# Optimization experiments

Hardware: AMD Instinct MI355X
Metric: run time of the kernel (lower is better)

## Reference

```python
import jax, jax.numpy as jnp
import numpy as np

B, N, D, F, L, R = 16, 1024, 256, 128, 2, 2


def setup_inputs() -> dict:
    key = jax.random.key(0)
    ks = jax.random.split(key, 12)
    s = 0.05
    return {
        "node_embed": jax.random.normal(ks[0], (B, N, D), jnp.float32),
        "input_x": jax.random.normal(ks[1], (B, F), jnp.float32),
        "adj": jax.random.randint(ks[2], (R, B, N, N), 0, 2, jnp.int32),
        "WQi_w": jax.random.normal(ks[3], (L, F, F), jnp.float32) * s,
        "WQi_b": jnp.zeros((L, F), jnp.float32),
        "WQ_w": jax.random.normal(ks[4], (L, D + F, D), jnp.float32) * s,
        "WQ_b": jnp.zeros((L, D), jnp.float32),
        "WK_w": jax.random.normal(ks[5], (L, R, D + F, D), jnp.float32) * s,
        "WK_b": jnp.zeros((L, R, D), jnp.float32),
        "WV_w": jax.random.normal(ks[6], (L, R, D + F, D), jnp.float32) * s,
        "WV_b": jnp.zeros((L, R, D), jnp.float32),
        "WF_w": jax.random.normal(ks[7], (L, R * D, D), jnp.float32) * s,
        "WF_b": jnp.zeros((L, D), jnp.float32),
        "ln_g": jnp.ones((L, D), jnp.float32),
        "ln_b": jnp.zeros((L, D), jnp.float32),
    }


def _layer_norm(x, g, b, eps=1e-5):
    mu = jnp.mean(x, axis=-1, keepdims=True)
    var = jnp.var(x, axis=-1, keepdims=True)
    return (x - mu) * jax.lax.rsqrt(var + eps) * g + b


def reference(node_embed, input_x, adj, WQi_w, WQi_b, WQ_w, WQ_b,
              WK_w, WK_b, WV_w, WV_b, WF_w, WF_b, ln_g, ln_b):
    scale = 1.0 / (D ** 0.5)
    h = node_embed
    for l in range(L):
        # input feature projection, broadcast over nodes
        x1 = input_x @ WQi_w[l] + WQi_b[l]              # (B, F)
        x1 = jnp.broadcast_to(x1[:, None, :], (h.shape[0], h.shape[1], F))
        qc = jnp.concatenate([h, x1], axis=-1)          # (B, N, D+F)
        q = qc @ WQ_w[l] + WQ_b[l]                      # (B, N, D)
        outs = []
        for r in range(R):
            k = qc @ WK_w[l, r] + WK_b[l, r]            # (B, N, D)
            v = qc @ WV_w[l, r] + WV_b[l, r]            # (B, N, D)
            scores = jnp.einsum('bnd,bmd->bnm', q, k) * scale
            scores = jnp.where(adj[r] == 0, -1e9, scores)
            alpha = jax.nn.softmax(scores, axis=-1)
            outs.append(jnp.einsum('bnm,bmd->bnd', alpha, v))
        h_concat = jnp.concatenate(outs, axis=-1)       # (B, N, R*D)
        h_fused = jax.nn.relu(h_concat @ WF_w[l] + WF_b[l])
        h = _layer_norm(h + h_fused, ln_g[l], ln_b[l])
    return h
```

## Files before the change

kernel.cpp:

```cpp
#include <hip/hip_runtime.h>
#include <hip/hip_bf16.h>

#define BB 16
#define NN 1024
#define DD 256
#define FF_ 128
#define LL 2
#define RR 2
#define DF 384
#define MM (BB*NN)
#define NPROJ 1280

typedef __attribute__((ext_vector_type(8))) short s16x8;
typedef __attribute__((ext_vector_type(4))) float f32x4;

__device__ __forceinline__ unsigned short f2bf(float f){
  unsigned u = __builtin_bit_cast(unsigned, f);
  u += 0x7fff + ((u >> 16) & 1);
  return (unsigned short)(u >> 16);
}

__device__ __forceinline__ void gload16(const void* g, void* l){
  __builtin_amdgcn_global_load_lds(
      (const __attribute__((address_space(1))) unsigned int*)g,
      (__attribute__((address_space(3))) unsigned int*)l, 16, 0, 0);
}

#define MFMA16(a,b,c) __builtin_amdgcn_mfma_f32_16x16x32_bf16((a),(b),(c),0,0,0)

__global__ __launch_bounds__(256) void pack_adj(const int* __restrict__ adj,
                                                unsigned long long* __restrict__ bits){
  int w = threadIdx.x >> 6, lane = threadIdx.x & 63;
  size_t row = (size_t)blockIdx.x * 4 + w;
  const int* a = adj + row * NN;
  unsigned long long* brow = bits + row * 16;
  #pragma unroll
  for (int j = 0; j < 16; ++j){
    unsigned long long m = __ballot(a[j*64 + lane] != 0);
    if (lane == 0) brow[j] = m;
  }
}

__global__ void x1_proj(const float* __restrict__ x, const float* __restrict__ wq,
                        const float* __restrict__ bq, float* __restrict__ x1){
  int b = blockIdx.x, j = threadIdx.x;
  float s = bq[j];
  for (int i = 0; i < FF_; ++i) s += x[b*FF_ + i] * wq[i*FF_ + j];
  x1[b*FF_ + j] = s;
}

__global__ void w_to_bf16T(const float* __restrict__ in, unsigned short* __restrict__ out, int K){
  int o = blockIdx.x * 256 + threadIdx.x;
  int n = o / K, k = o - n*K;
  out[o] = f2bf(in[(size_t)k * 256 + n]);
}

__global__ void wcat(const float* __restrict__ WQ, const float* __restrict__ WK,
                     const float* __restrict__ WV, unsigned short* __restrict__ wt){
  int o = blockIdx.x * 256 + threadIdx.x;
  int n = o / DF, k = o - n*DF;
  float v;
  if (n < 256)      v = WQ[(size_t)k*256 + n];
  else if (n < 768) v = WK[(size_t)((n-256)>>8)*(DF*256) + (size_t)k*256 + ((n-256)&255)];
  else              v = WV[(size_t)((n-768)>>8)*(DF*256) + (size_t)k*256 + ((n-768)&255)];
  wt[o] = f2bf(v);
}

__global__ void bcat(const float* __restrict__ bq, const float* __restrict__ bk,
                     const float* __restrict__ bv, float* __restrict__ ball){
  int n = blockIdx.x * 256 + threadIdx.x;
  if (n >= NPROJ) return;
  ball[n] = (n < 256) ? bq[n] : (n < 768) ? bk[n-256] : bv[n-768];
}

__global__ __launch_bounds__(256) void qc_h(const float* __restrict__ h, unsigned short* __restrict__ qc){
  int o = blockIdx.x * 256 + threadIdx.x;
  int m = o >> 8, c = o & 255;
  qc[(size_t)m * DF + c] = f2bf(h[o]);
}

__global__ __launch_bounds__(256) void qc_x1(const float* __restrict__ x1, unsigned short* __restrict__ qc){
  int m = blockIdx.x * 2 + (threadIdx.x >> 7);
  int c = threadIdx.x & 127;
  qc[(size_t)m * DF + 256 + c] = f2bf(x1[(m >> 10) * FF_ + c]);
}

template<int OUTF32>
__global__ __launch_bounds__(256) void gemm2(const unsigned short* __restrict__ A, int lda,
    const unsigned short* __restrict__ Wt, const float* __restrict__ bias,
    void* __restrict__ out, int ldo, int nk){
  __shared__ unsigned short As[2][128*32];
  __shared__ unsigned short Bs[2][128*32];
  int t = threadIdx.x, lane = t & 63, w = t >> 6;
  int wr = w >> 1, wc = w & 1, l15 = lane & 15, lhi = lane >> 4;
  int bm = blockIdx.x, bn = blockIdx.y;
  f32x4 acc[4][4];
  #pragma unroll
  for (int m = 0; m < 4; ++m)
    #pragma unroll
    for (int n = 0; n < 4; ++n) acc[m][n] = (f32x4){0.f,0.f,0.f,0.f};

  auto STAGE = [&](int bufi, int kk){
    #pragma unroll
    for (int i = 0; i < 2; ++i){
      int base = w*2048 + i*1024;
      int off = base + lane*16;
      int row = off >> 6, cb = off & 63;
      gload16((const char*)A  + ((size_t)(bm*128 + row)*lda + kk*32)*2 + cb,
              (char*)As[bufi] + base);
      gload16((const char*)Wt + ((size_t)(bn*128 + row)*DF  + 0)*0 + ((size_t)(bn*128 + row)*lda + kk*32)*2 + cb,
              (char*)Bs[bufi] + base);
    }
  };

  STAGE(0, 0);
  __syncthreads();
  for (int kk = 0; kk < nk; ++kk){
    int cur = kk & 1;
    if (kk + 1 < nk) STAGE(cur ^ 1, kk + 1);
    s16x8 af[4], bfr[4];
    #pragma unroll
    for (int m = 0; m < 4; ++m) af[m]  = *(const s16x8*)&As[cur][(wr*64 + m*16 + l15)*32 + lhi*8];
    #pragma unroll
    for (int n = 0; n < 4; ++n) bfr[n] = *(const s16x8*)&Bs[cur][(wc*64 + n*16 + l15)*32 + lhi*8];
    #pragma unroll
    for (int m = 0; m < 4; ++m)
      #pragma unroll
      for (int n = 0; n < 4; ++n)
        acc[m][n] = MFMA16(af[m], bfr[n], acc[m][n]);
    __syncthreads();
  }

  #pragma unroll
  for (int n = 0; n < 4; ++n){
    int gn = bn*128 + wc*64 + n*16 + l15;
    float bv = bias[gn];
    #pragma unroll
    for (int m = 0; m < 4; ++m){
      int gm = bm*128 + wr*64 + m*16 + lhi*4;
      #pragma unroll
      for (int i = 0; i < 4; ++i){
        float v = acc[m][n][i] + bv;
        size_t o = (size_t)(gm + i) * ldo + gn;
        if (OUTF32) ((float*)out)[o] = v;
        else        ((unsigned short*)out)[o] = f2bf(v);
      }
    }
  }
}

__global__ __launch_bounds__(256) void transpose2(const unsigned short* __restrict__ P,
                                                  unsigned short* __restrict__ vt){
  __shared__ unsigned short tl[64][66];
  int z = blockIdx.z;
  int b = z & 15, r = z >> 4;
  int n0 = blockIdx.x*64, d0 = blockIdx.y*64;
  int t = threadIdx.x;
  #pragma unroll
  for (int it = 0; it < 16; ++it){
    int idx = t + it*256;
    int rr = idx >> 6, cc = idx & 63;
    tl[rr][cc] = P[(size_t)(b*NN + n0 + rr)*NPROJ + 768 + r*256 + d0 + cc];
  }
  __syncthreads();
  #pragma unroll
  for (int it = 0; it < 16; ++it){
    int idx = t + it*256;
    int rr = idx >> 6, cc = idx & 63;
    vt[((size_t)z*256 + d0 + rr)*NN + n0 + cc] = tl[cc][rr];
  }
}

__global__ __launch_bounds__(512, 2) void attn2(const unsigned short* __restrict__ P,
    const unsigned short* __restrict__ VT, const unsigned long long* __restrict__ bits,
    unsigned short* __restrict__ hc){
  __shared__ unsigned short Kt[64*256];
  __shared__ unsigned short Vt[256*64];
  __shared__ unsigned short Pl[8][16*72];
  int t = threadIdx.x, lane = t & 63, w = t >> 6, l15 = lane & 15, lhi = lane >> 4;
  int F = blockIdx.x;
  int xcd = F & 7, j = F >> 3;
  int qt = j & 7;
  int gidx = xcd*4 + (j >> 3);
  int b = gidx & 15, r = gidx >> 4;
  const float scale = 0.0625f;

  const unsigned short* Qb = P;
  size_t kcol = 256 + (size_t)r*256;
  const unsigned short* Vb = VT + ((size_t)(r*16 + b))*256*NN;

  s16x8 qf[8];
  {
    int qrow = qt*128 + w*16 + l15;
    const unsigned short* qp = Qb + ((size_t)(b*NN + qrow))*NPROJ + lhi*8;
    #pragma unroll
    for (int dc = 0; dc < 8; ++dc) qf[dc] = *(const s16x8*)(qp + dc*32);
  }

  f32x4 acc[16];
  #pragma unroll
  for (int i = 0; i < 16; ++i) acc[i] = (f32x4){0.f,0.f,0.f,0.f};
  float mrow[4] = {-1e30f,-1e30f,-1e30f,-1e30f};
  float lrow[4] = {0.f,0.f,0.f,0.f};
  size_t bitrow = ((size_t)(r*BB + b))*NN + qt*128 + w*16 + lhi*4;

  for (int kt = 0; kt < 16; ++kt){
    __syncthreads();
    #pragma unroll
    for (int i = 0; i < 4; ++i){
      int base = w*4096 + i*512;
      int off = base + lane*16;
      (void)off;
    }
    #pragma unroll
    for (int i = 0; i < 4; ++i){
      int base = w*4096 + i*1024;
      int off = base + lane*16;
      int row = off >> 9, cb = off & 511;
      int scb = cb ^ ((row & 7) << 4);
      gload16((const char*)P + ((size_t)(b*NN + kt*64 + row)*NPROJ + kcol)*2 + scb,
              (char*)Kt + base);
    }
    #pragma unroll
    for (int i = 0; i < 4; ++i){
      int base = w*4096 + i*1024;
      int off = base + lane*16;
      int row = off >> 7, cb = off & 127;
      int scb = cb ^ ((row & 7) << 4);
      gload16((const char*)Vb + ((size_t)row*NN + kt*64)*2 + scb,
              (char*)Vt + base);
    }
    __syncthreads();

    f32x4 sf[4];
    #pragma unroll
    for (int ks = 0; ks < 4; ++ks){
      sf[ks] = (f32x4){0.f,0.f,0.f,0.f};
      int krow = ks*16 + l15;
      #pragma unroll
      for (int dc = 0; dc < 8; ++dc){
        int bo = krow*512 + (((dc*32 + lhi*8)*2) ^ ((krow & 7) << 4));
        s16x8 kf = *(const s16x8*)((const char*)Kt + bo);
        sf[ks] = MFMA16(qf[dc], kf, sf[ks]);
      }
    }

    unsigned short* pw = &Pl[w][0];
    #pragma unroll
    for (int i = 0; i < 4; ++i){
      unsigned long long mwv = bits[(bitrow + i)*16 + kt];
      float sv[4]; float tm = -1e30f;
      #pragma unroll
      for (int ks = 0; ks < 4; ++ks){
        float s = sf[ks][i] * scale;
        bool on = (mwv >> (ks*16 + l15)) & 1ULL;
        s = on ? s : -1e9f;
        sv[ks] = s;
        tm = fmaxf(tm, s);
      }
      #pragma unroll
      for (int xm = 1; xm < 16; xm <<= 1) tm = fmaxf(tm, __shfl_xor(tm, xm));
      float mn = fmaxf(mrow[i], tm);
      float f = __expf(mrow[i] - mn);
      mrow[i] = mn;
      float rs = 0.f;
      #pragma unroll
      for (int ks = 0; ks < 4; ++ks){
        float e = __expf(sv[ks] - mn);
        pw[(lhi*4 + i)*72 + ks*16 + l15] = f2bf(e);
        rs += e;
      }
      #pragma unroll
      for (int xm = 1; xm < 16; xm <<= 1) rs += __shfl_xor(rs, xm);
      lrow[i] = lrow[i]*f + rs;
      #pragma unroll
      for (int dt = 0; dt < 16; ++dt) acc[dt][i] *= f;
    }

    s16x8 pa[2];
    #pragma unroll
    for (int kc = 0; kc < 2; ++kc)
      pa[kc] = *(const s16x8*)&pw[l15*72 + kc*32 + lhi*8];

    #pragma unroll
    for (int dt = 0; dt < 16; ++dt){
      int vrow = dt*16 + l15;
      #pragma unroll
      for (int kc = 0; kc < 2; ++kc){
        int bo = vrow*128 + (((kc*32 + lhi*8)*2) ^ ((vrow & 7) << 4));
        s16x8 vf = *(const s16x8*)((const char*)Vt + bo);
        acc[dt] = MFMA16(pa[kc], vf, acc[dt]);
      }
    }
  }

  #pragma unroll
  for (int i = 0; i < 4; ++i){
    float inv = 1.f / lrow[i];
    int q = qt*128 + w*16 + lhi*4 + i;
    unsigned short* hrow = hc + ((size_t)(b*NN + q))*(RR*DD) + r*DD;
    #pragma unroll
    for (int dt = 0; dt < 16; ++dt)
      hrow[dt*16 + l15] = f2bf(acc[dt][i] * inv);
  }
}

template<int WRITEQC>
__global__ __launch_bounds__(256) void ln_res2(const float* __restrict__ ff,
    const float* __restrict__ hin, const float* __restrict__ g,
    const float* __restrict__ bv, float* __restrict__ hout,
    unsigned short* __restrict__ qc){
  int w = threadIdx.x >> 6, lane = threadIdx.x & 63;
  size_t row = (size_t)blockIdx.x * 4 + w;
  f32x4 fv = *(const f32x4*)(ff  + row*DD + lane*4);
  f32x4 hv = *(const f32x4*)(hin + row*DD + lane*4);
  float x[4], s = 0.f, ss = 0.f;
  #pragma unroll
  for (int j = 0; j < 4; ++j){ x[j] = fmaxf(fv[j], 0.f) + hv[j]; s += x[j]; ss += x[j]*x[j]; }
  #pragma unroll
  for (int xm = 1; xm < 64; xm <<= 1){ s += __shfl_xor(s, xm); ss += __shfl_xor(ss, xm); }
  float mu = s * (1.f/256.f);
  float var = ss * (1.f/256.f) - mu*mu;
  float rstd = rsqrtf(var + 1e-5f);
  f32x4 o;
  #pragma unroll
  for (int j = 0; j < 4; ++j){ int c = lane*4 + j; o[j] = (x[j]-mu)*rstd*g[c] + bv[c]; }
  *(f32x4*)(hout + row*DD + lane*4) = o;
  if (WRITEQC){
    unsigned v0 = (unsigned)f2bf(o[0]) | ((unsigned)f2bf(o[1]) << 16);
    unsigned v1 = (unsigned)f2bf(o[2]) | ((unsigned)f2bf(o[3]) << 16);
    uint2 pv; pv.x = v0; pv.y = v1;
    *(uint2*)(qc + row*DF + lane*4) = pv;
  }
}

extern "C" void kernel_launch(void* const* d_in, const int* in_sizes, int n_in,
                              void* d_out, int out_size, void* d_ws, size_t ws_size,
                              hipStream_t stream){
  (void)in_sizes; (void)n_in; (void)out_size; (void)ws_size;
  const float* node  = (const float*)d_in[0];
  const float* inx   = (const float*)d_in[1];
  const int*   adj   = (const int*)d_in[2];
  const float* WQi_w = (const float*)d_in[3];
  const float* WQi_b = (const float*)d_in[4];
  const float* WQ_w  = (const float*)d_in[5];
  const float* WQ_b  = (const float*)d_in[6];
  const float* WK_w  = (const float*)d_in[7];
  const float* WK_b  = (const float*)d_in[8];
  const float* WV_w  = (const float*)d_in[9];
  const float* WV_b  = (const float*)d_in[10];
  const float* WF_w  = (const float*)d_in[11];
  const float* WF_b  = (const float*)d_in[12];
  const float* ln_g  = (const float*)d_in[13];
  const float* ln_b  = (const float*)d_in[14];
  float* hout = (float*)d_out;

  char* wsp = (char*)d_ws;
  auto alloc = [&](size_t n){ char* p = wsp; wsp += (n + 255) & ~(size_t)255; return p; };
  unsigned long long* bits = (unsigned long long*)alloc((size_t)RR*BB*NN*16*8);
  unsigned short* qc    = (unsigned short*)alloc((size_t)MM*DF*2);
  float*          x1    = (float*)alloc((size_t)BB*FF_*4);
  unsigned short* wtall = (unsigned short*)alloc((size_t)NPROJ*DF*2);
  float*          ball  = (float*)alloc((size_t)NPROJ*4);
  unsigned short* wtf   = (unsigned short*)alloc((size_t)DD*512*2);
  unsigned short* POUT  = (unsigned short*)alloc((size_t)MM*NPROJ*2);
  unsigned short* vtall = (unsigned short*)alloc((size_t)RR*BB*DD*NN*2);
  unsigned short* hc    = (unsigned short*)alloc((size_t)MM*512*2);
  float*          ffo   = (float*)alloc((size_t)MM*DD*4);

  pack_adj<<<RR*BB*NN/4, 256, 0, stream>>>(adj, bits);

  for (int l = 0; l < LL; ++l){
    x1_proj<<<BB, FF_, 0, stream>>>(inx, WQi_w + (size_t)l*FF_*FF_, WQi_b + l*FF_, x1);
    qc_x1<<<MM/2, 256, 0, stream>>>(x1, qc);
    if (l == 0) qc_h<<<MM, 256, 0, stream>>>(node, qc);

    wcat<<<NPROJ*DF/256, 256, 0, stream>>>(WQ_w + (size_t)l*DF*DD,
                                           WK_w + (size_t)l*RR*DF*DD,
                                           WV_w + (size_t)l*RR*DF*DD, wtall);
    bcat<<<5, 256, 0, stream>>>(WQ_b + l*DD, WK_b + (size_t)l*RR*DD, WV_b + (size_t)l*RR*DD, ball);
    w_to_bf16T<<<512, 256, 0, stream>>>(WF_w + (size_t)l*512*DD, wtf, 512);

    gemm2<0><<<dim3(128,10), 256, 0, stream>>>(qc, DF, wtall, ball, POUT, NPROJ, DF/32);

    transpose2<<<dim3(16,4,RR*BB), 256, 0, stream>>>(POUT, vtall);

    attn2<<<256, 512, 0, stream>>>(POUT, vtall, bits, hc);

    gemm2<1><<<dim3(128,2), 256, 0, stream>>>(hc, 512, wtf, WF_b + l*DD, ffo, DD, 512/32);

    const float* hsrc = l ? (const float*)hout : node;
    if (l == 0) ln_res2<1><<<MM/4, 256, 0, stream>>>(ffo, hsrc, ln_g, ln_b, hout, qc);
    else        ln_res2<0><<<MM/4, 256, 0, stream>>>(ffo, hsrc, ln_g + DD, ln_b + DD, hout, qc);
  }
}
```

Before: 344.2 us.

## Fuse prep kernels, write V transposed from GEMM, double-buffer attention tiles

```diff
diff --git a/kernel.cpp b/kernel.cpp
--- a/kernel.cpp
+++ b/kernel.cpp
@@ -10,9 +10,11 @@
 #define DF 384
 #define MM (BB*NN)
 #define NPROJ 1280
+#define PK 768
 
 typedef __attribute__((ext_vector_type(8))) short s16x8;
 typedef __attribute__((ext_vector_type(4))) float f32x4;
+typedef __attribute__((ext_vector_type(4))) unsigned short us16x4;
 
 __device__ __forceinline__ unsigned short f2bf(float f){
   unsigned u = __builtin_bit_cast(unsigned, f);
@@ -41,54 +43,298 @@
   }
 }
 
-__global__ void x1_proj(const float* __restrict__ x, const float* __restrict__ wq,
-                        const float* __restrict__ bq, float* __restrict__ x1){
-  int b = blockIdx.x, j = threadIdx.x;
-  float s = bq[j];
-  for (int i = 0; i < FF_; ++i) s += x[b*FF_ + i] * wq[i*FF_ + j];
-  x1[b*FF_ + j] = s;
-}
-
-__global__ void w_to_bf16T(const float* __restrict__ in, unsigned short* __restrict__ out, int K){
-  int o = blockIdx.x * 256 + threadIdx.x;
-  int n = o / K, k = o - n*K;
-  out[o] = f2bf(in[(size_t)k * 256 + n]);
-}
-
-__global__ void wcat(const float* __restrict__ WQ, const float* __restrict__ WK,
-                     const float* __restrict__ WV, unsigned short* __restrict__ wt){
-  int o = blockIdx.x * 256 + threadIdx.x;
-  int n = o / DF, k = o - n*DF;
-  float v;
-  if (n < 256)      v = WQ[(size_t)k*256 + n];
-  else if (n < 768) v = WK[(size_t)((n-256)>>8)*(DF*256) + (size_t)k*256 + ((n-256)&255)];
-  else              v = WV[(size_t)((n-768)>>8)*(DF*256) + (size_t)k*256 + ((n-768)&255)];
-  wt[o] = f2bf(v);
-}
-
-__global__ void bcat(const float* __restrict__ bq, const float* __restrict__ bk,
-                     const float* __restrict__ bv, float* __restrict__ ball){
-  int n = blockIdx.x * 256 + threadIdx.x;
-  if (n >= NPROJ) return;
-  ball[n] = (n < 256) ? bq[n] : (n < 768) ? bk[n-256] : bv[n-768];
-}
-
-__global__ __launch_bounds__(256) void qc_h(const float* __restrict__ h, unsigned short* __restrict__ qc){
-  int o = blockIdx.x * 256 + threadIdx.x;
-  int m = o >> 8, c = o & 255;
-  qc[(size_t)m * DF + c] = f2bf(h[o]);
-}
-
-__global__ __launch_bounds__(256) void qc_x1(const float* __restrict__ x1, unsigned short* __restrict__ qc){
-  int m = blockIdx.x * 2 + (threadIdx.x >> 7);
-  int c = threadIdx.x & 127;
-  qc[(size_t)m * DF + 256 + c] = f2bf(x1[(m >> 10) * FF_ + c]);
-}
-
-template<int OUTF32>
-__global__ __launch_bounds__(256) void gemm2(const unsigned short* __restrict__ A, int lda,
+#define PREP_WT   3840
+#define PREP_WTF  1024
+#define PREP_BALL 10
+#define PREP_X1   16
+#define PREP_H    2048
+#define PREP_TOT  (PREP_WT+PREP_WTF+PREP_BALL+PREP_X1+PREP_H)
+
+__global__ __launch_bounds__(256) void prep(
+    const float* __restrict__ node, const float* __restrict__ inx,
+    const float* __restrict__ WQi_w, const float* __restrict__ WQi_b,
+    const float* __restrict__ WQ_w, const float* __restrict__ WK_w,
+    const float* __restrict__ WV_w, const float* __restrict__ WQ_b,
+    const float* __restrict__ WK_b, const float* __restrict__ WV_b,
+    const float* __restrict__ WF_w,
+    unsigned short* __restrict__ wtall, unsigned short* __restrict__ wtf,
+    float* __restrict__ ball, unsigned short* __restrict__ x1bf,
+    unsigned short* __restrict__ hbf){
+  int bid = blockIdx.x, t = threadIdx.x;
+  if (bid < PREP_WT){
+    int o = bid*256 + t;
+    int l = o / (NPROJ*DF); int oo = o - l*(NPROJ*DF);
+    int n = oo / DF, k = oo - n*DF;
+    const float* WQ = WQ_w + (size_t)l*DF*256;
+    const float* WK = WK_w + (size_t)l*RR*DF*256;
+    const float* WV = WV_w + (size_t)l*RR*DF*256;
+    float v;
+    if (n < 256)      v = WQ[(size_t)k*256 + n];
+    else if (n < 768) v = WK[(size_t)((n-256)>>8)*(DF*256) + (size_t)k*256 + ((n-256)&255)];
+    else              v = WV[(size_t)((n-768)>>8)*(DF*256) + (size_t)k*256 + ((n-768)&255)];
+    wtall[o] = f2bf(v);
+  } else if (bid < PREP_WT + PREP_WTF){
+    int o = (bid - PREP_WT)*256 + t;
+    int l = o >> 17; int oo = o & 131071;
+    int n = oo >> 9, k = oo & 511;
+    wtf[o] = f2bf(WF_w[(size_t)l*512*256 + (size_t)k*256 + n]);
+  } else if (bid < PREP_WT + PREP_WTF + PREP_BALL){
+    int o = (bid - PREP_WT - PREP_WTF)*256 + t;
+    if (o < 2*NPROJ){
+      int l = o / NPROJ, n = o - l*NPROJ;
+      float v = (n < 256) ? WQ_b[l*256 + n]
+              : (n < 768) ? WK_b[(size_t)l*512 + (n-256)]
+                          : WV_b[(size_t)l*512 + (n-768)];
+      ball[o] = v;
+    }
+  } else if (bid < PREP_WT + PREP_WTF + PREP_BALL + PREP_X1){
+    int o = (bid - PREP_WT - PREP_WTF - PREP_BALL)*256 + t;
+    int l = o >> 11, bj = o & 2047;
+    int b = bj >> 7, j = bj & 127;
+    const float* w = WQi_w + (size_t)l*FF_*FF_;
+    float s = WQi_b[l*FF_ + j];
+    for (int i = 0; i < FF_; ++i) s += inx[b*FF_ + i] * w[i*FF_ + j];
+    x1bf[o] = f2bf(s);
+  } else {
+    int o = (bid - (PREP_TOT - PREP_H))*256 + t;
+    const float4* src = (const float4*)node + (size_t)o*2;
+    float4 a = src[0], c = src[1];
+    uint4 pk;
+    pk.x = (unsigned)f2bf(a.x) | ((unsigned)f2bf(a.y) << 16);
+    pk.y = (unsigned)f2bf(a.z) | ((unsigned)f2bf(a.w) << 16);
+    pk.z = (unsigned)f2bf(c.x) | ((unsigned)f2bf(c.y) << 16);
+    pk.w = (unsigned)f2bf(c.z) | ((unsigned)f2bf(c.w) << 16);
+    *(uint4*)(hbf + (size_t)o*8) = pk;
+  }
+}
+
+__global__ __launch_bounds__(256) void gemm_big(const unsigned short* __restrict__ hbf,
+    const unsigned short* __restrict__ x1l, const unsigned short* __restrict__ Wt,
+    const float* __restrict__ bias, unsigned short* __restrict__ POUT,
+    unsigned short* __restrict__ vtall){
+  __shared__ unsigned short As[2][128*32];
+  __shared__ unsigned short Bs[2][128*32];
+  int t = threadIdx.x, lane = t & 63, w = t >> 6;
+  int wr = w >> 1, wc = w & 1, l15 = lane & 15, lhi = lane >> 4;
+  int bm = blockIdx.x, bn = blockIdx.y, bb = bm >> 3;
+  f32x4 acc[4][4];
+  #pragma unroll
+  for (int m = 0; m < 4; ++m)
+    #pragma unroll
+    for (int n = 0; n < 4; ++n) acc[m][n] = (f32x4){0.f,0.f,0.f,0.f};
+
+  auto STAGE = [&](int bi, int kk){
+    #pragma unroll
+    for (int i = 0; i < 2; ++i){
+      int base = w*2048 + i*1024;
+      int off = base + lane*16;
+      int row = off >> 6, cb = off & 63;
+      const char* asrc = (kk < 8)
+        ? (const char*)hbf + ((size_t)(bm*128 + row)*256 + kk*32)*2 + cb
+        : (const char*)x1l + ((size_t)bb*128 + (kk-8)*32)*2 + cb;
+      gload16(asrc, (char*)As[bi] + base);
+      gload16((const char*)Wt + ((size_t)(bn*128 + row)*DF + kk*32)*2 + cb,
+              (char*)Bs[bi] + base);
+    }
+  };
+
+  STAGE(0, 0);
+  __syncthreads();
+  for (int kk = 0; kk < 12; ++kk){
+    int cur = kk & 1;
+    if (kk + 1 < 12) STAGE(cur ^ 1, kk + 1);
+    s16x8 af[4], bfr[4];
+    #pragma unroll
+    for (int m = 0; m < 4; ++m) af[m]  = *(const s16x8*)&As[cur][(wr*64 + m*16 + l15)*32 + lhi*8];
+    #pragma unroll
+    for (int n = 0; n < 4; ++n) bfr[n] = *(const s16x8*)&Bs[cur][(wc*64 + n*16 + l15)*32 + lhi*8];
+    __builtin_amdgcn_s_setprio(1);
+    #pragma unroll
+    for (int m = 0; m < 4; ++m)
+      #pragma unroll
+      for (int n = 0; n < 4; ++n)
+        acc[m][n] = MFMA16(af[m], bfr[n], acc[m][n]);
+    __builtin_amdgcn_s_setprio(0);
+    __syncthreads();
+  }
+
+  if (bn < 6){
+    #pragma unroll
+    for (int n = 0; n < 4; ++n){
+      int gn = bn*128 + wc*64 + n*16 + l15;
+      float bv = bias[gn];
+      #pragma unroll
+      for (int m = 0; m < 4; ++m){
+        int gm = bm*128 + wr*64 + m*16 + lhi*4;
+        #pragma unroll
+        for (int i = 0; i < 4; ++i)
+          POUT[(size_t)(gm + i)*PK + gn] = f2bf(acc[m][n][i] + bv);
+      }
+    }
+  } else {
+    #pragma unroll
+    for (int n = 0; n < 4; ++n){
+      int gn = bn*128 + wc*64 + n*16 + l15;
+      float bv = bias[gn];
+      int rv = gn - 768;
+      int r = rv >> 8, d = rv & 255;
+      #pragma unroll
+      for (int m = 0; m < 4; ++m){
+        int mb = (bm & 7)*128 + wr*64 + m*16 + lhi*4;
+        us16x4 pk;
+        #pragma unroll
+        for (int i = 0; i < 4; ++i) pk[i] = f2bf(acc[m][n][i] + bv);
+        *(us16x4*)(vtall + ((size_t)((r*16 + bb)*256 + d))*NN + mb) = pk;
+      }
+    }
+  }
+}
+
+__global__ __launch_bounds__(512, 2) void attn2(const unsigned short* __restrict__ P,
+    const unsigned short* __restrict__ VT, const unsigned long long* __restrict__ bits,
+    unsigned short* __restrict__ hc){
+  __shared__ unsigned short Kt[2][64*256];
+  __shared__ unsigned short Vt[2][256*64];
+  __shared__ unsigned short Pl[8][16*68];
+  int t = threadIdx.x, lane = t & 63, w = t >> 6, l15 = lane & 15, lhi = lane >> 4;
+  int F = blockIdx.x;
+  int xcd = F & 7, j = F >> 3;
+  int qt = j & 7;
+  int gidx = xcd*4 + (j >> 3);
+  int b = gidx & 15, r = gidx >> 4;
+  const float C = 0.09016844f;
+
+  size_t kcol = 256 + (size_t)r*256;
+  const unsigned short* Vb = VT + ((size_t)(r*16 + b))*256*NN;
+
+  s16x8 qf[8];
+  {
+    int qrow = qt*128 + w*16 + l15;
+    const unsigned short* qp = P + ((size_t)(b*NN + qrow))*PK + lhi*8;
+    #pragma unroll
+    for (int dc = 0; dc < 8; ++dc) qf[dc] = *(const s16x8*)(qp + dc*32);
+  }
+
+  f32x4 acc[16];
+  #pragma unroll
+  for (int i = 0; i < 16; ++i) acc[i] = (f32x4){0.f,0.f,0.f,0.f};
+  float mrow[4] = {-3e38f,-3e38f,-3e38f,-3e38f};
+  float lrow[4] = {0.f,0.f,0.f,0.f};
+  size_t bitrow = ((size_t)(r*BB + b))*NN + qt*128 + w*16 + lhi*4;
+
+  auto STAGE = [&](int bi, int kt){
+    #pragma unroll
+    for (int i = 0; i < 4; ++i){
+      int base = w*4096 + i*1024;
+      int off = base + lane*16;
+      int row = off >> 9, cb = off & 511;
+      int scb = cb ^ ((row & 7) << 4);
+      gload16((const char*)P + ((size_t)(b*NN + kt*64 + row)*PK + kcol)*2 + scb,
+              (char*)Kt[bi] + base);
+    }
+    #pragma unroll
+    for (int i = 0; i < 4; ++i){
+      int base = w*4096 + i*1024;
+      int off = base + lane*16;
+      int row = off >> 7, cb = off & 127;
+      int scb = cb ^ ((row & 7) << 4);
+      gload16((const char*)Vb + ((size_t)row*NN + kt*64)*2 + scb,
+              (char*)Vt[bi] + base);
+    }
+  };
+
+  STAGE(0, 0);
+  __syncthreads();
+
+  for (int kt = 0; kt < 16; ++kt){
+    int cur = kt & 1;
+    if (kt + 1 < 16) STAGE(cur ^ 1, kt + 1);
+
+    f32x4 sf[4];
+    #pragma unroll
+    for (int ks = 0; ks < 4; ++ks){
+      sf[ks] = (f32x4){0.f,0.f,0.f,0.f};
+      int krow = ks*16 + l15;
+      __builtin_amdgcn_s_setprio(1);
+      #pragma unroll
+      for (int dc = 0; dc < 8; ++dc){
+        int bo = krow*512 + (((dc*32 + lhi*8)*2) ^ ((krow & 7) << 4));
+        s16x8 kf = *(const s16x8*)((const char*)Kt[cur] + bo);
+        sf[ks] = MFMA16(qf[dc], kf, sf[ks]);
+      }
+      __builtin_amdgcn_s_setprio(0);
+    }
+
+    unsigned short* pw = &Pl[w][0];
+    #pragma unroll
+    for (int i = 0; i < 4; ++i){
+      unsigned long long mwv = bits[(bitrow + i)*16 + kt];
+      float sv[4]; float tm = -3e38f;
+      #pragma unroll
+      for (int ks = 0; ks < 4; ++ks){
+        float s = sf[ks][i] * C;
+        bool on = (mwv >> (ks*16 + l15)) & 1ULL;
+        s = on ? s : -1.443e9f;
+        sv[ks] = s;
+        tm = fmaxf(tm, s);
+      }
+      #pragma unroll
+      for (int xm = 1; xm < 16; xm <<= 1) tm = fmaxf(tm, __shfl_xor(tm, xm));
+      float mn = mrow[i];
+      if (tm > mn + 11.6f){
+        float f = exp2f(mn - tm);
+        mrow[i] = tm; mn = tm;
+        lrow[i] *= f;
+        #pragma unroll
+        for (int dt = 0; dt < 16; ++dt) acc[dt][i] *= f;
+      }
+      float rs = 0.f;
+      #pragma unroll
+      for (int ks = 0; ks < 4; ++ks){
+        float e = exp2f(sv[ks] - mn);
+        pw[(lhi*4 + i)*68 + ks*16 + l15] = f2bf(e);
+        rs += e;
+      }
+      #pragma unroll
+      for (int xm = 1; xm < 16; xm <<= 1) rs += __shfl_xor(rs, xm);
+      lrow[i] += rs;
+    }
+
+    s16x8 pa[2];
+    #pragma unroll
+    for (int kc = 0; kc < 2; ++kc)
+      pa[kc] = *(const s16x8*)&pw[l15*68 + kc*32 + lhi*8];
+
+    __builtin_amdgcn_s_setprio(1);
+    #pragma unroll
+    for (int dt = 0; dt < 16; ++dt){
+      int vrow = dt*16 + l15;
+      #pragma unroll
+      for (int kc = 0; kc < 2; ++kc){
+        int bo = vrow*128 + (((kc*32 + lhi*8)*2) ^ ((vrow & 7) << 4));
+        s16x8 vf = *(const s16x8*)((const char*)Vt[cur] + bo);
+        acc[dt] = MFMA16(pa[kc], vf, acc[dt]);
+      }
+    }
+    __builtin_amdgcn_s_setprio(0);
+
+    __syncthreads();
+  }
+
+  #pragma unroll
+  for (int i = 0; i < 4; ++i){
+    float inv = 1.f / lrow[i];
+    int q = qt*128 + w*16 + lhi*4 + i;
+    unsigned short* hrow = hc + ((size_t)(b*NN + q))*(RR*DD) + r*DD;
+    #pragma unroll
+    for (int dt = 0; dt < 16; ++dt)
+      hrow[dt*16 + l15] = f2bf(acc[dt][i] * inv);
+  }
+}
+
+__global__ __launch_bounds__(256) void gemm_ff(const unsigned short* __restrict__ A,
     const unsigned short* __restrict__ Wt, const float* __restrict__ bias,
-    void* __restrict__ out, int ldo, int nk){
+    float* __restrict__ out){
   __shared__ unsigned short As[2][128*32];
   __shared__ unsigned short Bs[2][128*32];
   int t = threadIdx.x, lane = t & 63, w = t >> 6;
@@ -100,34 +346,36 @@
     #pragma unroll
     for (int n = 0; n < 4; ++n) acc[m][n] = (f32x4){0.f,0.f,0.f,0.f};
 
-  auto STAGE = [&](int bufi, int kk){
+  auto STAGE = [&](int bi, int kk){
     #pragma unroll
     for (int i = 0; i < 2; ++i){
       int base = w*2048 + i*1024;
       int off = base + lane*16;
       int row = off >> 6, cb = off & 63;
-      gload16((const char*)A  + ((size_t)(bm*128 + row)*lda + kk*32)*2 + cb,
-              (char*)As[bufi] + base);
-      gload16((const char*)Wt + ((size_t)(bn*128 + row)*DF  + 0)*0 + ((size_t)(bn*128 + row)*lda + kk*32)*2 + cb,
-              (char*)Bs[bufi] + base);
+      gload16((const char*)A  + ((size_t)(bm*128 + row)*512 + kk*32)*2 + cb,
+              (char*)As[bi] + base);
+      gload16((const char*)Wt + ((size_t)(bn*128 + row)*512 + kk*32)*2 + cb,
+              (char*)Bs[bi] + base);
     }
   };
 
   STAGE(0, 0);
   __syncthreads();
-  for (int kk = 0; kk < nk; ++kk){
+  for (int kk = 0; kk < 16; ++kk){
     int cur = kk & 1;
-    if (kk + 1 < nk) STAGE(cur ^ 1, kk + 1);
+    if (kk + 1 < 16) STAGE(cur ^ 1, kk + 1);
     s16x8 af[4], bfr[4];
     #pragma unroll
     for (int m = 0; m < 4; ++m) af[m]  = *(const s16x8*)&As[cur][(wr*64 + m*16 + l15)*32 + lhi*8];
     #pragma unroll
     for (int n = 0; n < 4; ++n) bfr[n] = *(const s16x8*)&Bs[cur][(wc*64 + n*16 + l15)*32 + lhi*8];
+    __builtin_amdgcn_s_setprio(1);
     #pragma unroll
     for (int m = 0; m < 4; ++m)
       #pragma unroll
       for (int n = 0; n < 4; ++n)
         acc[m][n] = MFMA16(af[m], bfr[n], acc[m][n]);
+    __builtin_amdgcn_s_setprio(0);
     __syncthreads();
   }
 
@@ -139,177 +387,17 @@
     for (int m = 0; m < 4; ++m){
       int gm = bm*128 + wr*64 + m*16 + lhi*4;
       #pragma unroll
-      for (int i = 0; i < 4; ++i){
-        float v = acc[m][n][i] + bv;
-        size_t o = (size_t)(gm + i) * ldo + gn;
-        if (OUTF32) ((float*)out)[o] = v;
-        else        ((unsigned short*)out)[o] = f2bf(v);
-      }
-    }
-  }
-}
-
-__global__ __launch_bounds__(256) void transpose2(const unsigned short* __restrict__ P,
-                                                  unsigned short* __restrict__ vt){
-  __shared__ unsigned short tl[64][66];
-  int z = blockIdx.z;
-  int b = z & 15, r = z >> 4;
-  int n0 = blockIdx.x*64, d0 = blockIdx.y*64;
-  int t = threadIdx.x;
-  #pragma unroll
-  for (int it = 0; it < 16; ++it){
-    int idx = t + it*256;
-    int rr = idx >> 6, cc = idx & 63;
-    tl[rr][cc] = P[(size_t)(b*NN + n0 + rr)*NPROJ + 768 + r*256 + d0 + cc];
-  }
-  __syncthreads();
-  #pragma unroll
-  for (int it = 0; it < 16; ++it){
-    int idx = t + it*256;
-    int rr = idx >> 6, cc = idx & 63;
-    vt[((size_t)z*256 + d0 + rr)*NN + n0 + cc] = tl[cc][rr];
-  }
-}
-
-__global__ __launch_bounds__(512, 2) void attn2(const unsigned short* __restrict__ P,
-    const unsigned short* __restrict__ VT, const unsigned long long* __restrict__ bits,
-    unsigned short* __restrict__ hc){
-  __shared__ unsigned short Kt[64*256];
-  __shared__ unsigned short Vt[256*64];
-  __shared__ unsigned short Pl[8][16*72];
-  int t = threadIdx.x, lane = t & 63, w = t >> 6, l15 = lane & 15, lhi = lane >> 4;
-  int F = blockIdx.x;
-  int xcd = F & 7, j = F >> 3;
-  int qt = j & 7;
-  int gidx = xcd*4 + (j >> 3);
-  int b = gidx & 15, r = gidx >> 4;
-  const float scale = 0.0625f;
-
-  const unsigned short* Qb = P;
-  size_t kcol = 256 + (size_t)r*256;
-  const unsigned short* Vb = VT + ((size_t)(r*16 + b))*256*NN;
-
-  s16x8 qf[8];
-  {
-    int qrow = qt*128 + w*16 + l15;
-    const unsigned short* qp = Qb + ((size_t)(b*NN + qrow))*NPROJ + lhi*8;
-    #pragma unroll
-    for (int dc = 0; dc < 8; ++dc) qf[dc] = *(const s16x8*)(qp + dc*32);
-  }
-
-  f32x4 acc[16];
-  #pragma unroll
-  for (int i = 0; i < 16; ++i) acc[i] = (f32x4){0.f,0.f,0.f,0.f};
-  float mrow[4] = {-1e30f,-1e30f,-1e30f,-1e30f};
-  float lrow[4] = {0.f,0.f,0.f,0.f};
-  size_t bitrow = ((size_t)(r*BB + b))*NN + qt*128 + w*16 + lhi*4;
-
-  for (int kt = 0; kt < 16; ++kt){
-    __syncthreads();
-    #pragma unroll
-    for (int i = 0; i < 4; ++i){
-      int base = w*4096 + i*512;
-      int off = base + lane*16;
-      (void)off;
-    }
-    #pragma unroll
-    for (int i = 0; i < 4; ++i){
-      int base = w*4096 + i*1024;
-      int off = base + lane*16;
-      int row = off >> 9, cb = off & 511;
-      int scb = cb ^ ((row & 7) << 4);
-      gload16((const char*)P + ((size_t)(b*NN + kt*64 + row)*NPROJ + kcol)*2 + scb,
-              (char*)Kt + base);
-    }
-    #pragma unroll
-    for (int i = 0; i < 4; ++i){
-      int base = w*4096 + i*1024;
-      int off = base + lane*16;
-      int row = off >> 7, cb = off & 127;
-      int scb = cb ^ ((row & 7) << 4);
-      gload16((const char*)Vb + ((size_t)row*NN + kt*64)*2 + scb,
-              (char*)Vt + base);
-    }
-    __syncthreads();
-
-    f32x4 sf[4];
-    #pragma unroll
-    for (int ks = 0; ks < 4; ++ks){
-      sf[ks] = (f32x4){0.f,0.f,0.f,0.f};
-      int krow = ks*16 + l15;
-      #pragma unroll
-      for (int dc = 0; dc < 8; ++dc){
-        int bo = krow*512 + (((dc*32 + lhi*8)*2) ^ ((krow & 7) << 4));
-        s16x8 kf = *(const s16x8*)((const char*)Kt + bo);
-        sf[ks] = MFMA16(qf[dc], kf, sf[ks]);
-      }
-    }
-
-    unsigned short* pw = &Pl[w][0];
-    #pragma unroll
-    for (int i = 0; i < 4; ++i){
-      unsigned long long mwv = bits[(bitrow + i)*16 + kt];
-      float sv[4]; float tm = -1e30f;
-      #pragma unroll
-      for (int ks = 0; ks < 4; ++ks){
-        float s = sf[ks][i] * scale;
-        bool on = (mwv >> (ks*16 + l15)) & 1ULL;
-        s = on ? s : -1e9f;
-        sv[ks] = s;
-        tm = fmaxf(tm, s);
-      }
-      #pragma unroll
-      for (int xm = 1; xm < 16; xm <<= 1) tm = fmaxf(tm, __shfl_xor(tm, xm));
-      float mn = fmaxf(mrow[i], tm);
-      float f = __expf(mrow[i] - mn);
-      mrow[i] = mn;
-      float rs = 0.f;
-      #pragma unroll
-      for (int ks = 0; ks < 4; ++ks){
-        float e = __expf(sv[ks] - mn);
-        pw[(lhi*4 + i)*72 + ks*16 + l15] = f2bf(e);
-        rs += e;
-      }
-      #pragma unroll
-      for (int xm = 1; xm < 16; xm <<= 1) rs += __shfl_xor(rs, xm);
-      lrow[i] = lrow[i]*f + rs;
-      #pragma unroll
-      for (int dt = 0; dt < 16; ++dt) acc[dt][i] *= f;
-    }
-
-    s16x8 pa[2];
-    #pragma unroll
-    for (int kc = 0; kc < 2; ++kc)
-      pa[kc] = *(const s16x8*)&pw[l15*72 + kc*32 + lhi*8];
-
-    #pragma unroll
-    for (int dt = 0; dt < 16; ++dt){
-      int vrow = dt*16 + l15;
-      #pragma unroll
-      for (int kc = 0; kc < 2; ++kc){
-        int bo = vrow*128 + (((kc*32 + lhi*8)*2) ^ ((vrow & 7) << 4));
-        s16x8 vf = *(const s16x8*)((const char*)Vt + bo);
-        acc[dt] = MFMA16(pa[kc], vf, acc[dt]);
-      }
-    }
-  }
-
-  #pragma unroll
-  for (int i = 0; i < 4; ++i){
-    float inv = 1.f / lrow[i];
-    int q = qt*128 + w*16 + lhi*4 + i;
-    unsigned short* hrow = hc + ((size_t)(b*NN + q))*(RR*DD) + r*DD;
-    #pragma unroll
-    for (int dt = 0; dt < 16; ++dt)
-      hrow[dt*16 + l15] = f2bf(acc[dt][i] * inv);
-  }
-}
-
-template<int WRITEQC>
+      for (int i = 0; i < 4; ++i)
+        out[(size_t)(gm + i)*DD + gn] = acc[m][n][i] + bv;
+    }
+  }
+}
+
+template<int WRITEH>
 __global__ __launch_bounds__(256) void ln_res2(const float* __restrict__ ff,
     const float* __restrict__ hin, const float* __restrict__ g,
     const float* __restrict__ bv, float* __restrict__ hout,
-    unsigned short* __restrict__ qc){
+    unsigned short* __restrict__ hbf){
   int w = threadIdx.x >> 6, lane = threadIdx.x & 63;
   size_t row = (size_t)blockIdx.x * 4 + w;
   f32x4 fv = *(const f32x4*)(ff  + row*DD + lane*4);
@@ -326,11 +414,11 @@
   #pragma unroll
   for (int j = 0; j < 4; ++j){ int c = lane*4 + j; o[j] = (x[j]-mu)*rstd*g[c] + bv[c]; }
   *(f32x4*)(hout + row*DD + lane*4) = o;
-  if (WRITEQC){
-    unsigned v0 = (unsigned)f2bf(o[0]) | ((unsigned)f2bf(o[1]) << 16);
-    unsigned v1 = (unsigned)f2bf(o[2]) | ((unsigned)f2bf(o[3]) << 16);
-    uint2 pv; pv.x = v0; pv.y = v1;
-    *(uint2*)(qc + row*DF + lane*4) = pv;
+  if (WRITEH){
+    uint2 pv;
+    pv.x = (unsigned)f2bf(o[0]) | ((unsigned)f2bf(o[1]) << 16);
+    pv.y = (unsigned)f2bf(o[2]) | ((unsigned)f2bf(o[3]) << 16);
+    *(uint2*)(hbf + row*DD + lane*4) = pv;
   }
 }
 
@@ -358,39 +446,31 @@
   char* wsp = (char*)d_ws;
   auto alloc = [&](size_t n){ char* p = wsp; wsp += (n + 255) & ~(size_t)255; return p; };
   unsigned long long* bits = (unsigned long long*)alloc((size_t)RR*BB*NN*16*8);
-  unsigned short* qc    = (unsigned short*)alloc((size_t)MM*DF*2);
-  float*          x1    = (float*)alloc((size_t)BB*FF_*4);
-  unsigned short* wtall = (unsigned short*)alloc((size_t)NPROJ*DF*2);
-  float*          ball  = (float*)alloc((size_t)NPROJ*4);
-  unsigned short* wtf   = (unsigned short*)alloc((size_t)DD*512*2);
-  unsigned short* POUT  = (unsigned short*)alloc((size_t)MM*NPROJ*2);
+  unsigned short* wtall = (unsigned short*)alloc((size_t)2*NPROJ*DF*2);
+  unsigned short* wtf   = (unsigned short*)alloc((size_t)2*DD*512*2);
+  float*          ball  = (float*)alloc((size_t)2*NPROJ*4);
+  unsigned short* x1bf  = (unsigned short*)alloc((size_t)2*BB*FF_*2);
+  unsigned short* hbf   = (unsigned short*)alloc((size_t)MM*DD*2);
+  unsigned short* POUT  = (unsigned short*)alloc((size_t)MM*PK*2);
   unsigned short* vtall = (unsigned short*)alloc((size_t)RR*BB*DD*NN*2);
   unsigned short* hc    = (unsigned short*)alloc((size_t)MM*512*2);
   float*          ffo   = (float*)alloc((size_t)MM*DD*4);
 
   pack_adj<<<RR*BB*NN/4, 256, 0, stream>>>(adj, bits);
+  prep<<<PREP_TOT, 256, 0, stream>>>(node, inx, WQi_w, WQi_b, WQ_w, WK_w, WV_w,
+                                     WQ_b, WK_b, WV_b, WF_w,
+                                     wtall, wtf, ball, x1bf, hbf);
 
   for (int l = 0; l < LL; ++l){
-    x1_proj<<<BB, FF_, 0, stream>>>(inx, WQi_w + (size_t)l*FF_*FF_, WQi_b + l*FF_, x1);
-    qc_x1<<<MM/2, 256, 0, stream>>>(x1, qc);
-    if (l == 0) qc_h<<<MM, 256, 0, stream>>>(node, qc);
-
-    wcat<<<NPROJ*DF/256, 256, 0, stream>>>(WQ_w + (size_t)l*DF*DD,
-                                           WK_w + (size_t)l*RR*DF*DD,
-                                           WV_w + (size_t)l*RR*DF*DD, wtall);
-    bcat<<<5, 256, 0, stream>>>(WQ_b + l*DD, WK_b + (size_t)l*RR*DD, WV_b + (size_t)l*RR*DD, ball);
-    w_to_bf16T<<<512, 256, 0, stream>>>(WF_w + (size_t)l*512*DD, wtf, 512);
-
-    gemm2<0><<<dim3(128,10), 256, 0, stream>>>(qc, DF, wtall, ball, POUT, NPROJ, DF/32);
-
-    transpose2<<<dim3(16,4,RR*BB), 256, 0, stream>>>(POUT, vtall);
+    gemm_big<<<dim3(128,10), 256, 0, stream>>>(hbf, x1bf + (size_t)l*BB*FF_,
+        wtall + (size_t)l*NPROJ*DF, ball + (size_t)l*NPROJ, POUT, vtall);
 
     attn2<<<256, 512, 0, stream>>>(POUT, vtall, bits, hc);
 
-    gemm2<1><<<dim3(128,2), 256, 0, stream>>>(hc, 512, wtf, WF_b + l*DD, ffo, DD, 512/32);
-
-    const float* hsrc = l ? (const float*)hout : node;
-    if (l == 0) ln_res2<1><<<MM/4, 256, 0, stream>>>(ffo, hsrc, ln_g, ln_b, hout, qc);
-    else        ln_res2<0><<<MM/4, 256, 0, stream>>>(ffo, hsrc, ln_g + DD, ln_b + DD, hout, qc);
-  }
-}
+    gemm_ff<<<dim3(128,2), 256, 0, stream>>>(hc, wtf + (size_t)l*DD*512, WF_b + l*DD, ffo);
+
+    if (l == 0) ln_res2<1><<<MM/4, 256, 0, stream>>>(ffo, node, ln_g, ln_b, hout, hbf);
+    else        ln_res2<0><<<MM/4, 256, 0, stream>>>(ffo, (const float*)hout,
+                                                     ln_g + DD, ln_b + DD, hout, nullptr);
+  }
+}
```

Measured after the change: 315.9 us. -8.2%, faster.
